# Optimization experiments

Hardware: AMD Instinct MI355X
Metric: run time of the kernel (lower is better)

Reference implementation:

```python
import jax, jax.numpy as jnp
import numpy as np

B, L, D = 2, 2048, 1024
H, NL = 16, 8
DH = D // H  # 64


def setup_inputs() -> dict:
    key = jax.random.key(0)
    ks = jax.random.split(key, 16)
    s_d = 1.0 / np.sqrt(D)
    s_ff = 1.0 / np.sqrt(4 * D)
    f32 = jnp.float32
    return {
        "x": jax.random.normal(ks[0], (B, L, D), f32),
        "pe": jax.random.normal(ks[1], (L, D), f32) / 10.0,
        "wq": jax.random.normal(ks[2], (NL, D, D), f32) * s_d,
        "wk": jax.random.normal(ks[3], (NL, D, D), f32) * s_d,
        "wv": jax.random.normal(ks[4], (NL, D, D), f32) * s_d,
        "ln1_g": 1.0 + 0.02 * jax.random.normal(ks[5], (NL, D), f32),
        "ln1_b": 0.02 * jax.random.normal(ks[6], (NL, D), f32),
        "w1": jax.random.normal(ks[7], (NL, D, 4 * D), f32) * s_d,
        "b1": jax.random.normal(ks[8], (NL, 4 * D), f32) * s_d,
        "w2": jax.random.normal(ks[9], (NL, 4 * D, D), f32) * s_ff,
        "b2": jax.random.normal(ks[10], (NL, D), f32) * s_ff,
        "ln2_g": 1.0 + 0.02 * jax.random.normal(ks[11], (NL, D), f32),
        "ln2_b": 0.02 * jax.random.normal(ks[12], (NL, D), f32),
    }


def _layernorm(x, g, b, eps=1e-5):
    m = jnp.mean(x, axis=-1, keepdims=True)
    v = jnp.mean(jnp.square(x - m), axis=-1, keepdims=True)
    return (x - m) * jax.lax.rsqrt(v + eps) * g + b


def reference(x, pe, wq, wk, wv, ln1_g, ln1_b, w1, b1, w2, b2, ln2_g, ln2_b):
    Bb, T, Dd = x.shape
    h = x + pe[:T]
    causal = jnp.tril(jnp.ones((T, T), dtype=bool))  # [T,T]
    inv_sqrt_dh = np.float32(1.0 / np.sqrt(DH))

    def step(h, p):
        wq_, wk_, wv_, g1, be1, w1_, bb1, w2_, bb2, g2, be2 = p
        # QKV: [B,T,D] -> [B,H,T,DH]
        q = (h @ wq_).reshape(Bb, T, H, DH).transpose(0, 2, 1, 3)
        k = (h @ wk_).reshape(Bb, T, H, DH).transpose(0, 2, 1, 3)
        v = (h @ wv_).reshape(Bb, T, H, DH).transpose(0, 2, 1, 3)
        scores = jnp.einsum('bhqd,bhkd->bhqk', q, k)
        scores = jnp.where(causal, scores, -jnp.inf)
        attn = jax.nn.softmax(scores * inv_sqrt_dh, axis=-1)
        o = jnp.einsum('bhqk,bhkd->bhqd', attn, v)
        o = o.transpose(0, 2, 1, 3).reshape(Bb, T, Dd)
        h = _layernorm(h + o, g1, be1)
        mlp = jax.nn.selu(h @ w1_ + bb1) @ w2_ + bb2
        h = _layernorm(h + mlp, g2, be2)
        return h, None

    h, _ = jax.lax.scan(step, h, (wq, wk, wv, ln1_g, ln1_b, w1, b1, w2, b2, ln2_g, ln2_b))
    return h
```

## Files before the change

### kernel.cpp

```cpp
#include <hip/hip_runtime.h>
#include <stdint.h>

typedef unsigned short u16;
typedef __bf16 bf16x8 __attribute__((ext_vector_type(8)));
typedef __bf16 bf16x4 __attribute__((ext_vector_type(4)));
typedef float f32x4 __attribute__((ext_vector_type(4)));

__device__ __forceinline__ float b2f(u16 b) {
    return __builtin_bit_cast(float, ((unsigned)b) << 16);
}
__device__ __forceinline__ u16 f2b(float f) {
    unsigned u = __builtin_bit_cast(unsigned, f);
    return (u16)((u + 0x7fffu + ((u >> 16) & 1u)) >> 16);
}
__device__ __forceinline__ void async16(const void* g, void* l) {
    __builtin_amdgcn_global_load_lds((const __attribute__((address_space(1))) void*)g,
                                     (__attribute__((address_space(3))) void*)l, 16, 0, 0);
}

__global__ __launch_bounds__(256) void add_pe_kernel(const float* __restrict__ x,
                                                     const float* __restrict__ pe,
                                                     float* __restrict__ hf,
                                                     u16* __restrict__ hb) {
    const size_t i = ((size_t)blockIdx.x * 256 + threadIdx.x) * 4;
    float4 xv = *(const float4*)(x + i);
    float4 pv = *(const float4*)(pe + (i & 2097151));
    float4 f;
    f.x = xv.x + pv.x; f.y = xv.y + pv.y; f.z = xv.z + pv.z; f.w = xv.w + pv.w;
    *(float4*)(hf + i) = f;
    ushort4 hv;
    hv.x = f2b(f.x); hv.y = f2b(f.y); hv.z = f2b(f.z); hv.w = f2b(f.w);
    *(ushort4*)(hb + i) = hv;
}

__global__ __launch_bounds__(256) void transpose_cast_kernel(const float* __restrict__ src,
                                                             u16* __restrict__ dst,
                                                             int srcStride, int K) {
    __shared__ __align__(16) u16 tile[64 * 72];
    const int n0 = blockIdx.x * 64, k0 = blockIdx.y * 64;
    const int t = threadIdx.x;
    const int r = t >> 3, c8 = (t & 7) * 8;
#pragma unroll
    for (int ph = 0; ph < 2; ph++) {
        const int rr = r + ph * 32;
        const float* s = src + (size_t)(k0 + rr) * srcStride + n0 + c8;
        float4 a = *(const float4*)s;
        float4 b = *(const float4*)(s + 4);
        u16* tr = tile + rr * 72 + c8;
        tr[0] = f2b(a.x); tr[1] = f2b(a.y); tr[2] = f2b(a.z); tr[3] = f2b(a.w);
        tr[4] = f2b(b.x); tr[5] = f2b(b.y); tr[6] = f2b(b.z); tr[7] = f2b(b.w);
    }
    __syncthreads();
#pragma unroll
    for (int ph = 0; ph < 2; ph++) {
        const int rr = r + ph * 32;
        union { float4 f; u16 u[8]; } ov;
#pragma unroll
        for (int j = 0; j < 8; j++) ov.u[j] = tile[(c8 + j) * 72 + rr];
        *(float4*)(dst + (size_t)(n0 + rr) * K + k0 + c8) = ov.f;
    }
}

__global__ __launch_bounds__(256) void transpose_qkv_kernel(const float* __restrict__ wq,
                                                            const float* __restrict__ wk,
                                                            const float* __restrict__ wv,
                                                            u16* __restrict__ dst) {
    __shared__ __align__(16) u16 tile[64 * 72];
    const float* src = (blockIdx.z == 0) ? wq : (blockIdx.z == 1) ? wk : wv;
    u16* d = dst + (size_t)blockIdx.z * 1048576;
    const int n0 = blockIdx.x * 64, k0 = blockIdx.y * 64;
    const int t = threadIdx.x;
    const int r = t >> 3, c8 = (t & 7) * 8;
#pragma unroll
    for (int ph = 0; ph < 2; ph++) {
        const int rr = r + ph * 32;
        const float* s = src + (size_t)(k0 + rr) * 1024 + n0 + c8;
        float4 a = *(const float4*)s;
        float4 b = *(const float4*)(s + 4);
        u16* tr = tile + rr * 72 + c8;
        tr[0] = f2b(a.x); tr[1] = f2b(a.y); tr[2] = f2b(a.z); tr[3] = f2b(a.w);
        tr[4] = f2b(b.x); tr[5] = f2b(b.y); tr[6] = f2b(b.z); tr[7] = f2b(b.w);
    }
    __syncthreads();
#pragma unroll
    for (int ph = 0; ph < 2; ph++) {
        const int rr = r + ph * 32;
        union { float4 f; u16 u[8]; } ov;
#pragma unroll
        for (int j = 0; j < 8; j++) ov.u[j] = tile[(c8 + j) * 72 + rr];
        *(float4*)(d + (size_t)(n0 + rr) * 1024 + k0 + c8) = ov.f;
    }
}

__global__ __launch_bounds__(256) void transpose_v_kernel(const u16* __restrict__ src,
                                                          u16* __restrict__ dst) {
    __shared__ __align__(16) u16 tile[64 * 72];
    const int bh = blockIdx.y, t0 = blockIdx.x * 64;
    const int t = threadIdx.x;
    const int r = t >> 3, c8 = (t & 7) * 8;
    const size_t base = (size_t)bh * 131072;
#pragma unroll
    for (int ph = 0; ph < 2; ph++) {
        const int rr = r + ph * 32;
        *(float4*)(tile + rr * 72 + c8) = *(const float4*)(src + base + (size_t)(t0 + rr) * 64 + c8);
    }
    __syncthreads();
#pragma unroll
    for (int ph = 0; ph < 2; ph++) {
        const int rr = r + ph * 32;
        union { float4 f; u16 u[8]; } ov;
#pragma unroll
        for (int j = 0; j < 8; j++) ov.u[j] = tile[(c8 + j) * 72 + rr];
        *(float4*)(dst + base + (size_t)rr * 2048 + t0 + c8) = ov.f;
    }
}

template <int MODE, int MTILES>
__global__ __launch_bounds__(256, 2) void gemm_kernel(const u16* __restrict__ A,
                                                      const u16* __restrict__ BT,
                                                      const float* __restrict__ bias,
                                                      void* __restrict__ O0, void* __restrict__ O1,
                                                      void* __restrict__ O2, int N, int K) {
    __shared__ __align__(16) u16 As[MTILES * 32 * 32];
    __shared__ __align__(16) u16 Bs[128 * 32];
    const int tid = threadIdx.x;
    const int lane = tid & 63, w = tid >> 6, quad = lane >> 4, l15 = lane & 15;
    const int m0 = blockIdx.y * (MTILES * 32), n0 = blockIdx.x * 128;
    const int wm = w >> 1, wn = w & 1;

    f32x4 acc[MTILES][4] = {};

    const int srow = tid >> 2, scol = (tid & 3) * 8;
    const u16* Ag = A + (size_t)(m0 + srow) * K + scol;
    const u16* Bg = BT + (size_t)(n0 + srow) * K + scol;
    u16* Asd = As + tid * 8;
    u16* Bsd = Bs + tid * 8;
    const size_t half = (size_t)64 * K;

    for (int k0 = 0; k0 < K; k0 += 32) {
        __syncthreads();
#pragma unroll
        for (int i = 0; i < MTILES / 2; i++) async16(Ag + k0 + i * half, Asd + i * 2048);
        async16(Bg + k0, Bsd);
        async16(Bg + k0 + half, Bsd + 2048);
        __syncthreads();
        bf16x8 af[MTILES], bfr[4];
#pragma unroll
        for (int mt = 0; mt < MTILES; mt++)
            af[mt] = *(const bf16x8*)(As + (wm * (MTILES * 16) + mt * 16 + l15) * 32 + quad * 8);
#pragma unroll
        for (int nt = 0; nt < 4; nt++)
            bfr[nt] = *(const bf16x8*)(Bs + (wn * 64 + nt * 16 + l15) * 32 + quad * 8);
#pragma unroll
        for (int mt = 0; mt < MTILES; mt++)
#pragma unroll
            for (int nt = 0; nt < 4; nt++)
                acc[mt][nt] = __builtin_amdgcn_mfma_f32_16x16x32_bf16(af[mt], bfr[nt], acc[mt][nt], 0, 0, 0);
    }

#pragma unroll
    for (int nt = 0; nt < 4; nt++) {
        const int col = n0 + wn * 64 + nt * 16 + l15;
        float bv = 0.f;
        if (MODE == 1 || MODE == 2) bv = bias[col];
#pragma unroll
        for (int mt = 0; mt < MTILES; mt++) {
#pragma unroll
            for (int r = 0; r < 4; r++) {
                const int row = m0 + wm * (MTILES * 16) + mt * 16 + quad * 4 + r;
                float val = acc[mt][nt][r];
                if (MODE == 0) {
                    const int mat = col >> 10, cc = col & 1023;
                    const int head = cc >> 6, dh = cc & 63;
                    const int b = row >> 11, t = row & 2047;
                    if (mat == 0) val *= 0.18033688f;
                    u16* dst = (mat == 0) ? (u16*)O0 : (mat == 1) ? (u16*)O1 : (u16*)O2;
                    dst[(((size_t)(b * 16 + head)) * 2048 + t) * 64 + dh] = f2b(val);
                } else if (MODE == 1) {
                    val += bv;
                    const float s = 1.0507009873554805f, a = 1.6732632423543772f;
                    val = val > 0.f ? s * val : s * a * (__expf(val) - 1.f);
                    ((u16*)O0)[(size_t)row * N + col] = f2b(val);
                } else if (MODE == 2) {
                    ((float*)O0)[(size_t)row * N + col] = val + bv;
                } else {
                    ((float*)O0)[(size_t)row * N + col] += val;
                }
            }
        }
    }
}

__global__ __launch_bounds__(256) void attn_kernel(const u16* __restrict__ q,
                                                   const u16* __restrict__ k,
                                                   const u16* __restrict__ vT,
                                                   u16* __restrict__ o) {
    __shared__ __align__(16) u16 Kt[64 * 72];
    __shared__ __align__(16) u16 Vt[64 * 72];
    __shared__ __align__(16) u16 Pt[4][32 * 72];
    const int tid = threadIdx.x, lane = tid & 63, w = tid >> 6, quad = lane >> 4, l15 = lane & 15;
    const int bh = blockIdx.x;
    const int qt = 15 - blockIdx.y;
    const size_t base = (size_t)bh * 131072;
    const int wrow0 = qt * 128 + w * 32;

    bf16x8 qf[2][2];
#pragma unroll
    for (int nt = 0; nt < 2; nt++)
#pragma unroll
        for (int ks = 0; ks < 2; ks++)
            qf[nt][ks] = *(const bf16x8*)(q + base + (size_t)(wrow0 + nt * 16 + l15) * 64 + ks * 32 + quad * 8);

    float m_[2], l_[2];
    m_[0] = m_[1] = -1e30f;
    l_[0] = l_[1] = 0.f;
    f32x4 oacc[2][4] = {};

    const int ktmax = (qt + 1) * 2;
    const int srow = tid >> 3, sc8 = (tid & 7) * 8;

    for (int kt = 0; kt < ktmax; kt++) {
        __syncthreads();
#pragma unroll
        for (int ph = 0; ph < 2; ph++) {
            const int rr = srow + ph * 32;
            *(float4*)(Kt + rr * 72 + sc8) = *(const float4*)(k + base + (size_t)(kt * 64 + rr) * 64 + sc8);
            *(float4*)(Vt + rr * 72 + sc8) = *(const float4*)(vT + base + (size_t)rr * 2048 + kt * 64 + sc8);
        }
        __syncthreads();
        const bool act = (kt * 64 <= wrow0 + 31);
        if (act) {
            f32x4 st[4][2];
#pragma unroll
            for (int mt = 0; mt < 4; mt++) {
                bf16x8 kf0 = *(const bf16x8*)(Kt + (mt * 16 + l15) * 72 + quad * 8);
                bf16x8 kf1 = *(const bf16x8*)(Kt + (mt * 16 + l15) * 72 + 32 + quad * 8);
#pragma unroll
                for (int nt = 0; nt < 2; nt++) {
                    f32x4 z = {};
                    z = __builtin_amdgcn_mfma_f32_16x16x32_bf16(kf0, qf[nt][0], z, 0, 0, 0);
                    z = __builtin_amdgcn_mfma_f32_16x16x32_bf16(kf1, qf[nt][1], z, 0, 0, 0);
                    st[mt][nt] = z;
                }
            }
            const bool needmask = (kt * 64 + 63 > wrow0);
            float alpha[2];
#pragma unroll
            for (int nt = 0; nt < 2; nt++) {
                const int qg = wrow0 + nt * 16 + l15;
                float mx = -1e30f;
                if (needmask) {
#pragma unroll
                    for (int mt = 0; mt < 4; mt++)
#pragma unroll
                        for (int r = 0; r < 4; r++) {
                            const int kg = kt * 64 + mt * 16 + quad * 4 + r;
                            float s = (kg <= qg) ? st[mt][nt][r] : -1e30f;
                            st[mt][nt][r] = s;
                            mx = fmaxf(mx, s);
                        }
                } else {
#pragma unroll
                    for (int mt = 0; mt < 4; mt++)
#pragma unroll
                        for (int r = 0; r < 4; r++) mx = fmaxf(mx, st[mt][nt][r]);
                }
                mx = fmaxf(mx, __shfl_xor(mx, 16, 64));
                mx = fmaxf(mx, __shfl_xor(mx, 32, 64));
                const float mnew = fmaxf(m_[nt], mx);
                alpha[nt] = exp2f(m_[nt] - mnew);
                m_[nt] = mnew;
                float rs = 0.f;
#pragma unroll
                for (int mt = 0; mt < 4; mt++) {
                    float p0 = exp2f(st[mt][nt][0] - mnew);
                    float p1 = exp2f(st[mt][nt][1] - mnew);
                    float p2 = exp2f(st[mt][nt][2] - mnew);
                    float p3 = exp2f(st[mt][nt][3] - mnew);
                    rs += (p0 + p1) + (p2 + p3);
                    bf16x4 pk = {(__bf16)p0, (__bf16)p1, (__bf16)p2, (__bf16)p3};
                    *(bf16x4*)(Pt[w] + (nt * 16 + l15) * 72 + mt * 16 + quad * 4) = pk;
                }
                rs += __shfl_xor(rs, 16, 64);
                rs += __shfl_xor(rs, 32, 64);
                l_[nt] = l_[nt] * alpha[nt] + rs;
            }
            float arow[2][4];
#pragma unroll
            for (int mto = 0; mto < 2; mto++)
#pragma unroll
                for (int r = 0; r < 4; r++)
                    arow[mto][r] = __shfl(alpha[mto], quad * 4 + r, 64);
#pragma unroll
            for (int mto = 0; mto < 2; mto++)
#pragma unroll
                for (int ntv = 0; ntv < 4; ntv++)
#pragma unroll
                    for (int r = 0; r < 4; r++) oacc[mto][ntv][r] *= arow[mto][r];

            bf16x8 pf[2][2];
#pragma unroll
            for (int mto = 0; mto < 2; mto++)
#pragma unroll
                for (int ks = 0; ks < 2; ks++)
                    pf[mto][ks] = *(const bf16x8*)(Pt[w] + (mto * 16 + l15) * 72 + ks * 32 + quad * 8);
#pragma unroll
            for (int ntv = 0; ntv < 4; ntv++) {
                bf16x8 vf0 = *(const bf16x8*)(Vt + (ntv * 16 + l15) * 72 + quad * 8);
                bf16x8 vf1 = *(const bf16x8*)(Vt + (ntv * 16 + l15) * 72 + 32 + quad * 8);
#pragma unroll
                for (int mto = 0; mto < 2; mto++) {
                    oacc[mto][ntv] = __builtin_amdgcn_mfma_f32_16x16x32_bf16(pf[mto][0], vf0, oacc[mto][ntv], 0, 0, 0);
                    oacc[mto][ntv] = __builtin_amdgcn_mfma_f32_16x16x32_bf16(pf[mto][1], vf1, oacc[mto][ntv], 0, 0, 0);
                }
            }
        }
    }

    float linv[2] = {1.f / l_[0], 1.f / l_[1]};
    float rinv[2][4];
#pragma unroll
    for (int mto = 0; mto < 2; mto++)
#pragma unroll
        for (int r = 0; r < 4; r++)
            rinv[mto][r] = __shfl(linv[mto], quad * 4 + r, 64);

    const int b = bh >> 4, hh = bh & 15;
#pragma unroll
    for (int mto = 0; mto < 2; mto++)
#pragma unroll
        for (int ntv = 0; ntv < 4; ntv++)
#pragma unroll
            for (int r = 0; r < 4; r++) {
                const int trow = wrow0 + mto * 16 + quad * 4 + r;
                const int col = hh * 64 + ntv * 16 + l15;
                o[((size_t)b * 2048 + trow) * 1024 + col] = f2b(oacc[mto][ntv][r] * rinv[mto][r]);
            }
}

template <int ADD_BF16>
__global__ __launch_bounds__(256) void ln_kernel(const float* __restrict__ hin,
                                                 const void* __restrict__ addp,
                                                 const float* __restrict__ g,
                                                 const float* __restrict__ bt,
                                                 float* __restrict__ hf_out,
                                                 u16* __restrict__ hb_out) {
    const int w = threadIdx.x >> 6, lane = threadIdx.x & 63;
    const size_t row = (size_t)blockIdx.x * 4 + w;
    const float4* hr = (const float4*)(hin + row * 1024);
    float4 xv[4];
    float s = 0.f, s2 = 0.f;
#pragma unroll
    for (int j = 0; j < 4; j++) {
        const int idx = lane + 64 * j;
        float4 a = hr[idx];
        float4 b;
        if (ADD_BF16) {
            ushort4 av = ((const ushort4*)addp)[row * 256 + idx];
            b.x = b2f(av.x); b.y = b2f(av.y); b.z = b2f(av.z); b.w = b2f(av.w);
        } else {
            b = ((const float4*)addp)[row * 256 + idx];
        }
        float4 x;
        x.x = a.x + b.x; x.y = a.y + b.y; x.z = a.z + b.z; x.w = a.w + b.w;
        xv[j] = x;
        s += x.x + x.y + x.z + x.w;
        s2 += x.x * x.x + x.y * x.y + x.z * x.z + x.w * x.w;
    }
#pragma unroll
    for (int mm = 1; mm < 64; mm <<= 1) { s += __shfl_xor(s, mm, 64); s2 += __shfl_xor(s2, mm, 64); }
    const float mean = s * (1.f / 1024.f);
    const float var = s2 * (1.f / 1024.f) - mean * mean;
    const float rstd = rsqrtf(var + 1e-5f);
    float4* of = (float4*)(hf_out + row * 1024);
    ushort4* ob = (ushort4*)(hb_out + row * 1024);
    const float4* gv = (const float4*)g;
    const float4* bv = (const float4*)bt;
#pragma unroll
    for (int j = 0; j < 4; j++) {
        const int idx = lane + 64 * j;
        float4 gg = gv[idx], bb = bv[idx];
        float4 x = xv[j], y;
        y.x = (x.x - mean) * rstd * gg.x + bb.x;
        y.y = (x.y - mean) * rstd * gg.y + bb.y;
        y.z = (x.z - mean) * rstd * gg.z + bb.z;
        y.w = (x.w - mean) * rstd * gg.w + bb.w;
        of[idx] = y;
        ushort4 oo;
        oo.x = f2b(y.x); oo.y = f2b(y.y); oo.z = f2b(y.z); oo.w = f2b(y.w);
        ob[idx] = oo;
    }
}

extern "C" void kernel_launch(void* const* d_in, const int* in_sizes, int n_in,
                              void* d_out, int out_size, void* d_ws, size_t ws_size,
                              hipStream_t stream) {
    const float* x   = (const float*)d_in[0];
    const float* pe  = (const float*)d_in[1];
    const float* wq  = (const float*)d_in[2];
    const float* wk  = (const float*)d_in[3];
    const float* wv  = (const float*)d_in[4];
    const float* l1g = (const float*)d_in[5];
    const float* l1b = (const float*)d_in[6];
    const float* w1  = (const float*)d_in[7];
    const float* b1  = (const float*)d_in[8];
    const float* w2  = (const float*)d_in[9];
    const float* b2  = (const float*)d_in[10];
    const float* l2g = (const float*)d_in[11];
    const float* l2b = (const float*)d_in[12];

    char* ws = (char*)d_ws;
    float* hf   = (float*)(ws);
    u16* hb     = (u16*)(ws + 16777216);
    u16* qb     = (u16*)(ws + 25165824);
    u16* kb     = (u16*)(ws + 33554432);
    u16* vb     = (u16*)(ws + 41943040);
    u16* wqkvT  = (u16*)(ws + 50331648);
    u16* vbt    = (u16*)(ws + 50331648);
    u16* ob     = (u16*)(ws + 41943040);
    u16* wslot  = (u16*)(ws + 25165824);
    u16* ub     = (u16*)(ws + 29360128);
    float* mb   = (float*)(ws + 46137344);

    add_pe_kernel<<<4096, 256, 0, stream>>>(x, pe, hf, hb);

    for (int l = 0; l < 8; l++) {
        transpose_qkv_kernel<<<dim3(16, 16, 3), 256, 0, stream>>>(
            wq + (size_t)l * 1048576, wk + (size_t)l * 1048576, wv + (size_t)l * 1048576, wqkvT);
        gemm_kernel<0, 4><<<dim3(24, 32), 256, 0, stream>>>(hb, wqkvT, nullptr, qb, kb, vb, 3072, 1024);
        transpose_v_kernel<<<dim3(32, 32), 256, 0, stream>>>(vb, vbt);
        attn_kernel<<<dim3(32, 16), 256, 0, stream>>>(qb, kb, vbt, ob);
        ln_kernel<1><<<1024, 256, 0, stream>>>(hf, ob, l1g + l * 1024, l1b + l * 1024, hf, hb);
        for (int half = 0; half < 2; half++) {
            transpose_cast_kernel<<<dim3(32, 16), 256, 0, stream>>>(
                w1 + (size_t)l * 4194304 + half * 2048, wslot, 4096, 1024);
            gemm_kernel<1, 4><<<dim3(16, 32), 256, 0, stream>>>(
                hb, wslot, b1 + l * 4096 + half * 2048, ub, nullptr, nullptr, 2048, 1024);
            transpose_cast_kernel<<<dim3(16, 32), 256, 0, stream>>>(
                w2 + (size_t)l * 4194304 + (size_t)half * 2048 * 1024, wslot, 1024, 2048);
            if (half == 0)
                gemm_kernel<2, 2><<<dim3(8, 64), 256, 0, stream>>>(
                    ub, wslot, b2 + l * 1024, mb, nullptr, nullptr, 1024, 2048);
            else
                gemm_kernel<3, 2><<<dim3(8, 64), 256, 0, stream>>>(
                    ub, wslot, nullptr, mb, nullptr, nullptr, 1024, 2048);
        }
        const bool last = (l == 7);
        ln_kernel<0><<<1024, 256, 0, stream>>>(hf, mb, l2g + l * 1024, l2b + l * 1024,
                                               last ? (float*)d_out : hf, hb);
    }
}
```

Baseline: 2.519 ms.

## Add 256x256 pipelined GEMM kernel and unsplit the MLP into full-width GEMMs

Adds a 512-thread GEMM kernel with 256x256 output tiles, double-buffered async global-to-LDS loads with a swizzled layout, staggered prefetch between MFMA phases, and setprio/sched barriers. It is used for the QKV projection and the first MLP GEMM. The MLP is no longer split into two halves: W1 and W2 are transposed whole into separate workspace regions, so the second GEMM runs once over K=4096 instead of in two accumulate passes. The goal is more operand reuse per tile, fewer launches and less fp32 read-modify-write traffic, at the cost of a larger workspace and fewer blocks per grid (192 and 256 blocks) on a many-CU GPU.

New measurement: 2.290 ms. -9.1%, faster.

```diff
diff --git a/kernel.cpp b/kernel.cpp
--- a/kernel.cpp
+++ b/kernel.cpp
@@ -169,14 +169,7 @@
             for (int r = 0; r < 4; r++) {
                 const int row = m0 + wm * (MTILES * 16) + mt * 16 + quad * 4 + r;
                 float val = acc[mt][nt][r];
-                if (MODE == 0) {
-                    const int mat = col >> 10, cc = col & 1023;
-                    const int head = cc >> 6, dh = cc & 63;
-                    const int b = row >> 11, t = row & 2047;
-                    if (mat == 0) val *= 0.18033688f;
-                    u16* dst = (mat == 0) ? (u16*)O0 : (mat == 1) ? (u16*)O1 : (u16*)O2;
-                    dst[(((size_t)(b * 16 + head)) * 2048 + t) * 64 + dh] = f2b(val);
-                } else if (MODE == 1) {
+                if (MODE == 1) {
                     val += bv;
                     const float s = 1.0507009873554805f, a = 1.6732632423543772f;
                     val = val > 0.f ? s * val : s * a * (__expf(val) - 1.f);
@@ -185,6 +178,149 @@
                     ((float*)O0)[(size_t)row * N + col] = val + bv;
                 } else {
                     ((float*)O0)[(size_t)row * N + col] += val;
+                }
+            }
+        }
+    }
+}
+
+#define G_SYNC1()                                          \
+    __builtin_amdgcn_sched_barrier(0);                     \
+    __builtin_amdgcn_s_barrier();                          \
+    asm volatile("s_waitcnt lgkmcnt(0)" ::: "memory");     \
+    __builtin_amdgcn_sched_barrier(0);                     \
+    __builtin_amdgcn_s_setprio(1)
+#define G_SYNC2()                                          \
+    __builtin_amdgcn_s_setprio(0);                         \
+    __builtin_amdgcn_sched_barrier(0);                     \
+    __builtin_amdgcn_s_barrier()
+
+template <int MODE, int NT>
+__global__ __launch_bounds__(512) void gemm256_kernel(const u16* __restrict__ A,
+                                                      const u16* __restrict__ BT,
+                                                      const float* __restrict__ bias,
+                                                      void* __restrict__ O0, void* __restrict__ O1,
+                                                      void* __restrict__ O2, int N) {
+    constexpr int K = NT * 64;
+    __shared__ __align__(16) u16 lds[65536];
+    const int tid = threadIdx.x;
+    const int lane = tid & 63, w = tid >> 6, quad = lane >> 4, l15 = lane & 15;
+    const int wm = w >> 2, wn = w & 3;
+    const int m0 = blockIdx.y * 256, n0 = blockIdx.x * 256;
+
+    f32x4 acc[8][4] = {};
+
+    const int srow = tid >> 2;
+    const int slog = (tid & 3) ^ ((tid >> 3) & 3);
+    const u16* pA = A + (size_t)(m0 + srow) * K + slog * 8;
+    const u16* pB = BT + (size_t)(n0 + srow) * K + slog * 8;
+    u16* const ldst = lds + tid * 8;
+
+    const int swz = (quad ^ ((l15 >> 1) & 3)) * 8;
+    const int aro = (wm * 128 + l15) * 32 + swz;
+    const int bro = 16384 + (wn * 64 + l15) * 32 + swz;
+
+    auto stA = [&](int tt, int kh) {
+        u16* d = ldst + ((tt & 1) << 15) + (kh << 13);
+        const u16* s = pA + tt * 64 + kh * 32;
+        async16(s, d);
+        async16(s + (size_t)128 * K, d + 4096);
+    };
+    auto stB = [&](int tt, int kh) {
+        u16* d = ldst + ((tt & 1) << 15) + 16384 + (kh << 13);
+        const u16* s = pB + tt * 64 + kh * 32;
+        async16(s, d);
+        async16(s + (size_t)128 * K, d + 4096);
+    };
+
+    stB(0, 0); stB(0, 1); stA(0, 0); stA(0, 1);
+    stB(1, 0); stB(1, 1); stA(1, 0);
+    asm volatile("s_waitcnt vmcnt(6)" ::: "memory");
+    __builtin_amdgcn_s_barrier();
+
+#pragma unroll 2
+    for (int t = 0; t < NT; ++t) {
+        const int boff = (t & 1) << 15;
+        bf16x8 a[4], bk0[4], bk1[4];
+#pragma unroll
+        for (int i = 0; i < 4; i++) a[i] = *(const bf16x8*)(lds + boff + aro + i * 512);
+#pragma unroll
+        for (int i = 0; i < 4; i++) bk0[i] = *(const bf16x8*)(lds + boff + bro + i * 512);
+        if (t + 1 < NT) stA(t + 1, 1);
+        G_SYNC1();
+#pragma unroll
+        for (int mt = 0; mt < 4; mt++)
+#pragma unroll
+            for (int nt = 0; nt < 4; nt++)
+                acc[mt][nt] = __builtin_amdgcn_mfma_f32_16x16x32_bf16(a[mt], bk0[nt], acc[mt][nt], 0, 0, 0);
+        G_SYNC2();
+#pragma unroll
+        for (int i = 0; i < 4; i++) a[i] = *(const bf16x8*)(lds + boff + 8192 + aro + i * 512);
+#pragma unroll
+        for (int i = 0; i < 4; i++) bk1[i] = *(const bf16x8*)(lds + boff + 8192 + bro + i * 512);
+        if (t + 2 < NT) stB(t + 2, 0);
+        G_SYNC1();
+#pragma unroll
+        for (int mt = 0; mt < 4; mt++)
+#pragma unroll
+            for (int nt = 0; nt < 4; nt++)
+                acc[mt][nt] = __builtin_amdgcn_mfma_f32_16x16x32_bf16(a[mt], bk1[nt], acc[mt][nt], 0, 0, 0);
+        G_SYNC2();
+#pragma unroll
+        for (int i = 0; i < 4; i++) a[i] = *(const bf16x8*)(lds + boff + aro + 2048 + i * 512);
+        if (t + 2 < NT) stB(t + 2, 1);
+        G_SYNC1();
+#pragma unroll
+        for (int mt = 0; mt < 4; mt++)
+#pragma unroll
+            for (int nt = 0; nt < 4; nt++)
+                acc[4 + mt][nt] = __builtin_amdgcn_mfma_f32_16x16x32_bf16(a[mt], bk0[nt], acc[4 + mt][nt], 0, 0, 0);
+        G_SYNC2();
+#pragma unroll
+        for (int i = 0; i < 4; i++) a[i] = *(const bf16x8*)(lds + boff + 8192 + aro + 2048 + i * 512);
+        if (t + 2 < NT) stA(t + 2, 0);
+        G_SYNC1();
+#pragma unroll
+        for (int mt = 0; mt < 4; mt++)
+#pragma unroll
+            for (int nt = 0; nt < 4; nt++)
+                acc[4 + mt][nt] = __builtin_amdgcn_mfma_f32_16x16x32_bf16(a[mt], bk1[nt], acc[4 + mt][nt], 0, 0, 0);
+        __builtin_amdgcn_s_setprio(0);
+        __builtin_amdgcn_sched_barrier(0);
+        if (t < NT - 2) {
+            asm volatile("s_waitcnt vmcnt(6)" ::: "memory");
+        } else if (t == NT - 2) {
+            asm volatile("s_waitcnt vmcnt(0)" ::: "memory");
+        }
+        __builtin_amdgcn_sched_barrier(0);
+        __builtin_amdgcn_s_barrier();
+    }
+
+#pragma unroll
+    for (int nt = 0; nt < 4; nt++) {
+        const int col = n0 + wn * 64 + nt * 16 + l15;
+        float bv = 0.f;
+        if (MODE == 1 || MODE == 2) bv = bias[col];
+#pragma unroll
+        for (int am = 0; am < 8; am++) {
+#pragma unroll
+            for (int r = 0; r < 4; r++) {
+                const int row = m0 + wm * 128 + am * 16 + quad * 4 + r;
+                float val = acc[am][nt][r];
+                if (MODE == 0) {
+                    const int mat = col >> 10, cc = col & 1023;
+                    const int head = cc >> 6, dh = cc & 63;
+                    const int b = row >> 11, tt = row & 2047;
+                    if (mat == 0) val *= 0.18033688f;
+                    u16* dst = (mat == 0) ? (u16*)O0 : (mat == 1) ? (u16*)O1 : (u16*)O2;
+                    dst[(((size_t)(b * 16 + head)) * 2048 + tt) * 64 + dh] = f2b(val);
+                } else if (MODE == 1) {
+                    val += bv;
+                    const float s = 1.0507009873554805f, aa = 1.6732632423543772f;
+                    val = val > 0.f ? s * val : s * aa * (__expf(val) - 1.f);
+                    ((u16*)O0)[(size_t)row * N + col] = f2b(val);
+                } else if (MODE == 2) {
+                    ((float*)O0)[(size_t)row * N + col] = val + bv;
                 }
             }
         }
@@ -415,36 +551,27 @@
     u16* qb     = (u16*)(ws + 25165824);
     u16* kb     = (u16*)(ws + 33554432);
     u16* vb     = (u16*)(ws + 41943040);
-    u16* wqkvT  = (u16*)(ws + 50331648);
     u16* vbt    = (u16*)(ws + 50331648);
     u16* ob     = (u16*)(ws + 41943040);
-    u16* wslot  = (u16*)(ws + 25165824);
-    u16* ub     = (u16*)(ws + 29360128);
-    float* mb   = (float*)(ws + 46137344);
+    u16* wqkvT  = (u16*)(ws + 58720256);
+    u16* w1T    = (u16*)(ws + 65011712);
+    u16* w2T    = (u16*)(ws + 73400320);
+    u16* ub     = (u16*)(ws + 81788928);
+    float* mb   = (float*)(ws + 115343360);
 
     add_pe_kernel<<<4096, 256, 0, stream>>>(x, pe, hf, hb);
 
     for (int l = 0; l < 8; l++) {
         transpose_qkv_kernel<<<dim3(16, 16, 3), 256, 0, stream>>>(
             wq + (size_t)l * 1048576, wk + (size_t)l * 1048576, wv + (size_t)l * 1048576, wqkvT);
-        gemm_kernel<0, 4><<<dim3(24, 32), 256, 0, stream>>>(hb, wqkvT, nullptr, qb, kb, vb, 3072, 1024);
+        gemm256_kernel<0, 16><<<dim3(12, 16), 512, 0, stream>>>(hb, wqkvT, nullptr, qb, kb, vb, 3072);
         transpose_v_kernel<<<dim3(32, 32), 256, 0, stream>>>(vb, vbt);
         attn_kernel<<<dim3(32, 16), 256, 0, stream>>>(qb, kb, vbt, ob);
         ln_kernel<1><<<1024, 256, 0, stream>>>(hf, ob, l1g + l * 1024, l1b + l * 1024, hf, hb);
-        for (int half = 0; half < 2; half++) {
-            transpose_cast_kernel<<<dim3(32, 16), 256, 0, stream>>>(
-                w1 + (size_t)l * 4194304 + half * 2048, wslot, 4096, 1024);
-            gemm_kernel<1, 4><<<dim3(16, 32), 256, 0, stream>>>(
-                hb, wslot, b1 + l * 4096 + half * 2048, ub, nullptr, nullptr, 2048, 1024);
-            transpose_cast_kernel<<<dim3(16, 32), 256, 0, stream>>>(
-                w2 + (size_t)l * 4194304 + (size_t)half * 2048 * 1024, wslot, 1024, 2048);
-            if (half == 0)
-                gemm_kernel<2, 2><<<dim3(8, 64), 256, 0, stream>>>(
-                    ub, wslot, b2 + l * 1024, mb, nullptr, nullptr, 1024, 2048);
-            else
-                gemm_kernel<3, 2><<<dim3(8, 64), 256, 0, stream>>>(
-                    ub, wslot, nullptr, mb, nullptr, nullptr, 1024, 2048);
-        }
+        transpose_cast_kernel<<<dim3(64, 16), 256, 0, stream>>>(w1 + (size_t)l * 4194304, w1T, 4096, 1024);
+        gemm256_kernel<1, 16><<<dim3(16, 16), 512, 0, stream>>>(hb, w1T, b1 + l * 4096, ub, nullptr, nullptr, 4096);
+        transpose_cast_kernel<<<dim3(16, 64), 256, 0, stream>>>(w2 + (size_t)l * 4194304, w2T, 1024, 4096);
+        gemm_kernel<2, 2><<<dim3(8, 64), 256, 0, stream>>>(ub, w2T, b2 + l * 1024, mb, nullptr, nullptr, 1024, 4096);
         const bool last = (l == 7);
         ln_kernel<0><<<1024, 256, 0, stream>>>(hf, mb, l2g + l * 1024, l2b + l * 1024,
                                                last ? (float*)d_out : hf, hb);
```
